# Kernel tuning notes

Measured on AMD Instinct MI355X. Metric: run time of the kernel, lower is better.

The kernel has to match this reference:

```python
import jax, jax.numpy as jnp
import numpy as np

N_BINS = 15
DELTA = 1.0 / N_BINS


def setup_inputs() -> dict:
    key = jax.random.key(0)
    k1, k2 = jax.random.split(key)
    N, C = 4_000_000, 10
    # scale 5 -> confident softmax -> low collision entropy so bins [0,1) are populated
    logits = jax.random.normal(k1, (N, C), dtype=jnp.float32) * 5.0
    labels = jax.random.randint(k2, (N,), 0, C)
    return {"logits": logits, "labels": labels}


def reference(logits, labels):
    # probs: [N, C]
    probs = jax.nn.softmax(logits, axis=-1)
    # collision entropy H2 per sample: [N]
    u = -jnp.log2(jnp.sum(probs * probs, axis=-1) + 1e-12)
    err_real = (jnp.argmax(probs, axis=-1) != labels).astype(jnp.float32)  # [N]

    n = u.shape[0]
    # bin b covers [b*DELTA, (b+1)*DELTA); samples with u outside [0,1) go to overflow bin
    bin_idx = jnp.floor(u / DELTA).astype(jnp.int32)
    valid = (u >= 0.0) & (u < 1.0)
    seg = jnp.where(valid, bin_idx, N_BINS)

    vf = valid.astype(jnp.float32)
    counts = jax.ops.segment_sum(vf, seg, num_segments=N_BINS + 1)[:N_BINS]
    sum_u = jax.ops.segment_sum(jnp.where(valid, u, 0.0), seg, num_segments=N_BINS + 1)[:N_BINS]
    sum_err = jax.ops.segment_sum(jnp.where(valid, err_real, 0.0), seg, num_segments=N_BINS + 1)[:N_BINS]

    pi = counts / n                      # population weight per bin
    nonempty = counts > 0
    cnt = jnp.where(nonempty, counts, 1.0)
    u_b = sum_u / cnt                    # mean H2 in bin
    err_b = sum_err / cnt                # empirical error rate in bin

    # risk-from-H2 reference curve
    inner = jnp.clip(2.0 * jnp.exp2(-u_b) - 1.0, 0.0, None)
    r_ref = 0.5 * (1.0 - jnp.sqrt(inner))

    gaps = jnp.where(nonempty, jnp.abs(err_b - r_ref) * pi, 0.0)
    return jnp.sum(gaps)
```

## Files before the change

kernel.cpp:

```cpp
#include <hip/hip_runtime.h>
#include <math.h>
#include <stdint.h>

#define NB 15
#define TROWS 512
#define TBYTES (TROWS * 40)
#define LBYTES (TROWS * 4)
#define NCOPY 8
#define ACCSTRIDE 64


__device__ __forceinline__ void gload_lds16(const void* g, void* ldsBase, uint32_t ldsByteOff)
{
    __builtin_amdgcn_global_load_lds(
        (const __attribute__((address_space(1))) uint32_t*)g,
        (__attribute__((address_space(3))) uint32_t*)((char*)ldsBase + ldsByteOff),
        16, 0, 0);
}

__device__ __forceinline__ void gload_lds4(const void* g, void* ldsBase, uint32_t ldsByteOff)
{
    __builtin_amdgcn_global_load_lds(
        (const __attribute__((address_space(1))) uint32_t*)g,
        (__attribute__((address_space(3))) uint32_t*)((char*)ldsBase + ldsByteOff),
        4, 0, 0);
}

__device__ __forceinline__ void row_stats(const float lv[10], float lvl_lab, bool rowOK,
                                          int& bin, float& u, int& e10)
{
    float m = lv[0];
#pragma unroll
    for (int j = 1; j < 10; ++j) m = fmaxf(m, lv[j]);

    const float c = 1.44269504088896340736f;
    float mc = m * c;
    float Z = 0.0f, S = 0.0f;
#pragma unroll
    for (int j = 0; j < 10; ++j) {
        float e = exp2f(fmaf(lv[j], c, -mc));
        Z += e;
        S = fmaf(e, e, S);
    }
    float ratio = S * __builtin_amdgcn_rcpf(Z * Z);
    u = -log2f(ratio + 1e-12f);

    bool valid = rowOK && (u >= 0.0f) && (u < 1.0f);
    bin = -1;
    if (valid) {
        bin = (int)(u * 15.0f);
        if (bin > 14) bin = 14;
    }
    if (!valid) u = 0.0f;
    e10 = (lvl_lab != m) ? 1 : 0;
}

__global__ __launch_bounds__(256) void bin_kernel(
    const float* __restrict__ logits,
    const int* __restrict__ labels,
    float* __restrict__ acc,
    int N, int numTiles)
{
    __shared__ float ldsLog[2][TROWS * 10];
    __shared__ int   ldsLab[2][TROWS];
    __shared__ float s_acc[3 * NB];

    const int t = threadIdx.x;
    if (t < 3 * NB) s_acc[t] = 0.0f;
    const int wid  = t >> 6;
    const int lane = t & 63;

    int   pk[NB];
    float su[NB];
#pragma unroll
    for (int b = 0; b < NB; ++b) { pk[b] = 0; su[b] = 0.0f; }

    const char* srcB = (const char*)logits;
    const char* labB = (const char*)labels;
    const long long totB  = (long long)N * 40;
    const long long ltotB = (long long)N * 4;

    auto stage = [&](int buf, long long tl) {
#pragma unroll
        for (int k = 0; k < 5; ++k) {
            uint32_t loff = (uint32_t)(wid * 5 + k) << 10;
            long long gb = tl * TBYTES + loff + lane * 16;
            if (gb > totB - 16) gb = totB - 16;
            gload_lds16(srcB + gb, &ldsLog[buf][0], __builtin_amdgcn_readfirstlane(loff));
        }
#pragma unroll
        for (int k = 0; k < 2; ++k) {
            uint32_t loff = (uint32_t)(wid * 2 + k) << 8;
            long long gb = tl * LBYTES + loff + lane * 4;
            if (gb > ltotB - 4) gb = ltotB - 4;
            gload_lds4(labB + gb, &ldsLab[buf][0], __builtin_amdgcn_readfirstlane(loff));
        }
    };

    long long tile = blockIdx.x;
    stage(0, tile);
    int cur = 0;

    for (; tile < numTiles; tile += gridDim.x) {
        const long long nxt = tile + gridDim.x;
        const bool hasNext = (nxt < numTiles);
        if (hasNext) {
            stage(cur ^ 1, nxt);
            asm volatile("s_waitcnt vmcnt(7)" ::: "memory");
        } else {
            asm volatile("s_waitcnt vmcnt(0)" ::: "memory");
        }
        __builtin_amdgcn_s_barrier();

        const float* L  = ldsLog[cur];
        const int*   LB = ldsLab[cur];

        const int r0 = (int)tile * TROWS + t;
        const int r1 = r0 + 256;
        int lab0 = LB[t];       lab0 = lab0 < 0 ? 0 : (lab0 > 9 ? 9 : lab0);
        int lab1 = LB[t + 256]; lab1 = lab1 < 0 ? 0 : (lab1 > 9 ? 9 : lab1);

        float a[10], b2[10];
        {
            const float2* p = (const float2*)(L + t * 10);
#pragma unroll
            for (int j = 0; j < 5; ++j) { float2 w = p[j]; a[2*j] = w.x; a[2*j+1] = w.y; }
        }
        {
            const float2* p = (const float2*)(L + (t + 256) * 10);
#pragma unroll
            for (int j = 0; j < 5; ++j) { float2 w = p[j]; b2[2*j] = w.x; b2[2*j+1] = w.y; }
        }
        float lvl0 = L[t * 10 + lab0];
        float lvl1 = L[(t + 256) * 10 + lab1];

        int binA, eA, binB, eB;
        float uA, uB;
        row_stats(a,  lvl0, r0 < N, binA, uA, eA);
        row_stats(b2, lvl1, r1 < N, binB, uB, eB);

        int incA = 1 + (eA << 16);
        int incB = 1 + (eB << 16);
#pragma unroll
        for (int b = 0; b < NB; ++b) {
            bool mA = (binA == b);
            bool mB = (binB == b);
            pk[b] += (mA ? incA : 0) + (mB ? incB : 0);
            su[b] += (mA ? uA : 0.0f) + (mB ? uB : 0.0f);
        }

        asm volatile("s_waitcnt lgkmcnt(0)" ::: "memory");
        __builtin_amdgcn_s_barrier();
        cur ^= 1;
    }

#pragma unroll
    for (int b = 0; b < NB; ++b) {
        int   p = pk[b];
        float s = su[b];
#pragma unroll
        for (int off = 1; off < 64; off <<= 1) {
            p += __shfl_xor(p, off, 64);
            s += __shfl_xor(s, off, 64);
        }
        if (lane == 0) {
            atomicAdd(&s_acc[b],          (float)(p & 0xFFFF));
            atomicAdd(&s_acc[NB + b],     s);
            atomicAdd(&s_acc[2 * NB + b], (float)(p >> 16));
        }
    }
    __syncthreads();
    if (t < 3 * NB) {
        float v = s_acc[t];
        if (v != 0.0f)
            atomicAdd(&acc[(blockIdx.x & (NCOPY - 1)) * ACCSTRIDE + t], v);
    }
}

__global__ void finalize_kernel(const float* __restrict__ acc,
                                float* __restrict__ out, float n)
{
    int b = threadIdx.x;
    float gap = 0.0f;
    if (b < NB) {
        float cnt = 0.0f, sumu = 0.0f, serr = 0.0f;
#pragma unroll
        for (int c = 0; c < NCOPY; ++c) {
            cnt  += acc[c * ACCSTRIDE + b];
            sumu += acc[c * ACCSTRIDE + NB + b];
            serr += acc[c * ACCSTRIDE + 2 * NB + b];
        }
        if (cnt > 0.0f) {
            float u_b   = sumu / cnt;
            float err_b = serr / cnt;
            float inner = 2.0f * exp2f(-u_b) - 1.0f;
            if (inner < 0.0f) inner = 0.0f;
            float r_ref = 0.5f * (1.0f - sqrtf(inner));
            gap = fabsf(err_b - r_ref) * (cnt / n);
        }
    }
#pragma unroll
    for (int off = 32; off >= 1; off >>= 1)
        gap += __shfl_xor(gap, off, 64);
    if (b == 0) out[0] = gap;
}

extern "C" void kernel_launch(void* const* d_in, const int* in_sizes, int n_in,
                              void* d_out, int out_size, void* d_ws, size_t ws_size,
                              hipStream_t stream)
{
    const float* logits = (const float*)d_in[0];
    const int*   labels = (const int*)d_in[1];
    const int N = in_sizes[1];

    float* acc = (float*)d_ws;
    hipMemsetAsync(acc, 0, NCOPY * ACCSTRIDE * sizeof(float), stream);

    const int numTiles = (N + TROWS - 1) / TROWS;
    int blocks = numTiles < 768 ? numTiles : 768;
    bin_kernel<<<blocks, 256, 0, stream>>>(logits, labels, acc, N, numTiles);
    finalize_kernel<<<1, 64, 0, stream>>>(acc, (float*)d_out, (float)N);
}
```

Measured before the change: 242.2 us.

## Replace LDS double-buffered staging with direct per-thread global loads

Removes the global_load_lds double-buffered tile staging and the per-tile barriers. Each thread now reads its own row straight from global memory with strided float2 loads in a grid-stride loop, and the label logit is picked with selects instead of an indexed LDS read. The grid grows from 768 to 1024 blocks. This drops the barrier and LDS overhead, but each thread's row reads are 40-byte strided and less coalesced, and there is no explicit prefetch.

```diff
diff --git a/kernel.cpp b/kernel.cpp
--- a/kernel.cpp
+++ b/kernel.cpp
@@ -3,71 +3,20 @@
 #include <stdint.h>
 
 #define NB 15
-#define TROWS 512
-#define TBYTES (TROWS * 40)
-#define LBYTES (TROWS * 4)
 #define NCOPY 8
 #define ACCSTRIDE 64
 
 
-__device__ __forceinline__ void gload_lds16(const void* g, void* ldsBase, uint32_t ldsByteOff)
-{
-    __builtin_amdgcn_global_load_lds(
-        (const __attribute__((address_space(1))) uint32_t*)g,
-        (__attribute__((address_space(3))) uint32_t*)((char*)ldsBase + ldsByteOff),
-        16, 0, 0);
-}
-
-__device__ __forceinline__ void gload_lds4(const void* g, void* ldsBase, uint32_t ldsByteOff)
-{
-    __builtin_amdgcn_global_load_lds(
-        (const __attribute__((address_space(1))) uint32_t*)g,
-        (__attribute__((address_space(3))) uint32_t*)((char*)ldsBase + ldsByteOff),
-        4, 0, 0);
-}
-
-__device__ __forceinline__ void row_stats(const float lv[10], float lvl_lab, bool rowOK,
-                                          int& bin, float& u, int& e10)
-{
-    float m = lv[0];
-#pragma unroll
-    for (int j = 1; j < 10; ++j) m = fmaxf(m, lv[j]);
-
-    const float c = 1.44269504088896340736f;
-    float mc = m * c;
-    float Z = 0.0f, S = 0.0f;
-#pragma unroll
-    for (int j = 0; j < 10; ++j) {
-        float e = exp2f(fmaf(lv[j], c, -mc));
-        Z += e;
-        S = fmaf(e, e, S);
-    }
-    float ratio = S * __builtin_amdgcn_rcpf(Z * Z);
-    u = -log2f(ratio + 1e-12f);
-
-    bool valid = rowOK && (u >= 0.0f) && (u < 1.0f);
-    bin = -1;
-    if (valid) {
-        bin = (int)(u * 15.0f);
-        if (bin > 14) bin = 14;
-    }
-    if (!valid) u = 0.0f;
-    e10 = (lvl_lab != m) ? 1 : 0;
-}
-
 __global__ __launch_bounds__(256) void bin_kernel(
     const float* __restrict__ logits,
     const int* __restrict__ labels,
-    float* __restrict__ acc,
-    int N, int numTiles)
+    float* __restrict__ acc, int N)
 {
-    __shared__ float ldsLog[2][TROWS * 10];
-    __shared__ int   ldsLab[2][TROWS];
     __shared__ float s_acc[3 * NB];
-
     const int t = threadIdx.x;
     if (t < 3 * NB) s_acc[t] = 0.0f;
-    const int wid  = t >> 6;
+    __syncthreads();
+
     const int lane = t & 63;
 
     int   pk[NB];
@@ -75,83 +24,51 @@
 #pragma unroll
     for (int b = 0; b < NB; ++b) { pk[b] = 0; su[b] = 0.0f; }
 
-    const char* srcB = (const char*)logits;
-    const char* labB = (const char*)labels;
-    const long long totB  = (long long)N * 40;
-    const long long ltotB = (long long)N * 4;
+    const long long stride = (long long)gridDim.x * 256;
 
-    auto stage = [&](int buf, long long tl) {
+    for (long long r = (long long)blockIdx.x * 256 + t; r < N; r += stride) {
+        const float2* p = (const float2*)(logits + r * 10);
+        float lv[10];
 #pragma unroll
-        for (int k = 0; k < 5; ++k) {
-            uint32_t loff = (uint32_t)(wid * 5 + k) << 10;
-            long long gb = tl * TBYTES + loff + lane * 16;
-            if (gb > totB - 16) gb = totB - 16;
-            gload_lds16(srcB + gb, &ldsLog[buf][0], __builtin_amdgcn_readfirstlane(loff));
+        for (int j = 0; j < 5; ++j) { float2 w = p[j]; lv[2*j] = w.x; lv[2*j+1] = w.y; }
+        const int lab = labels[r];
+
+        float lvl = lv[0];
+#pragma unroll
+        for (int j = 1; j < 10; ++j) lvl = (lab == j) ? lv[j] : lvl;
+
+        float m = lv[0];
+#pragma unroll
+        for (int j = 1; j < 10; ++j) m = fmaxf(m, lv[j]);
+
+        const float c = 1.44269504088896340736f;
+        float mc = m * c;
+        float Z = 0.0f, S = 0.0f;
+#pragma unroll
+        for (int j = 0; j < 10; ++j) {
+            float e = exp2f(fmaf(lv[j], c, -mc));
+            Z += e;
+            S = fmaf(e, e, S);
         }
-#pragma unroll
-        for (int k = 0; k < 2; ++k) {
-            uint32_t loff = (uint32_t)(wid * 2 + k) << 8;
-            long long gb = tl * LBYTES + loff + lane * 4;
-            if (gb > ltotB - 4) gb = ltotB - 4;
-            gload_lds4(labB + gb, &ldsLab[buf][0], __builtin_amdgcn_readfirstlane(loff));
+        float ratio = S * __builtin_amdgcn_rcpf(Z * Z);
+        float u = -log2f(ratio + 1e-12f);
+
+        bool valid = (u >= 0.0f) && (u < 1.0f);
+        int bin = -1;
+        if (valid) {
+            bin = (int)(u * 15.0f);
+            if (bin > 14) bin = 14;
         }
-    };
+        if (!valid) u = 0.0f;
+        int e10 = (lvl != m) ? 1 : 0;
+        int inc = 1 + (e10 << 16);
 
-    long long tile = blockIdx.x;
-    stage(0, tile);
-    int cur = 0;
-
-    for (; tile < numTiles; tile += gridDim.x) {
-        const long long nxt = tile + gridDim.x;
-        const bool hasNext = (nxt < numTiles);
-        if (hasNext) {
-            stage(cur ^ 1, nxt);
-            asm volatile("s_waitcnt vmcnt(7)" ::: "memory");
-        } else {
-            asm volatile("s_waitcnt vmcnt(0)" ::: "memory");
-        }
-        __builtin_amdgcn_s_barrier();
-
-        const float* L  = ldsLog[cur];
-        const int*   LB = ldsLab[cur];
-
-        const int r0 = (int)tile * TROWS + t;
-        const int r1 = r0 + 256;
-        int lab0 = LB[t];       lab0 = lab0 < 0 ? 0 : (lab0 > 9 ? 9 : lab0);
-        int lab1 = LB[t + 256]; lab1 = lab1 < 0 ? 0 : (lab1 > 9 ? 9 : lab1);
-
-        float a[10], b2[10];
-        {
-            const float2* p = (const float2*)(L + t * 10);
-#pragma unroll
-            for (int j = 0; j < 5; ++j) { float2 w = p[j]; a[2*j] = w.x; a[2*j+1] = w.y; }
-        }
-        {
-            const float2* p = (const float2*)(L + (t + 256) * 10);
-#pragma unroll
-            for (int j = 0; j < 5; ++j) { float2 w = p[j]; b2[2*j] = w.x; b2[2*j+1] = w.y; }
-        }
-        float lvl0 = L[t * 10 + lab0];
-        float lvl1 = L[(t + 256) * 10 + lab1];
-
-        int binA, eA, binB, eB;
-        float uA, uB;
-        row_stats(a,  lvl0, r0 < N, binA, uA, eA);
-        row_stats(b2, lvl1, r1 < N, binB, uB, eB);
-
-        int incA = 1 + (eA << 16);
-        int incB = 1 + (eB << 16);
 #pragma unroll
         for (int b = 0; b < NB; ++b) {
-            bool mA = (binA == b);
-            bool mB = (binB == b);
-            pk[b] += (mA ? incA : 0) + (mB ? incB : 0);
-            su[b] += (mA ? uA : 0.0f) + (mB ? uB : 0.0f);
+            bool mb = (bin == b);
+            pk[b] += mb ? inc : 0;
+            su[b] += mb ? u : 0.0f;
         }
-
-        asm volatile("s_waitcnt lgkmcnt(0)" ::: "memory");
-        __builtin_amdgcn_s_barrier();
-        cur ^= 1;
     }
 
 #pragma unroll
@@ -216,8 +133,9 @@
     float* acc = (float*)d_ws;
     hipMemsetAsync(acc, 0, NCOPY * ACCSTRIDE * sizeof(float), stream);
 
-    const int numTiles = (N + TROWS - 1) / TROWS;
-    int blocks = numTiles < 768 ? numTiles : 768;
-    bin_kernel<<<blocks, 256, 0, stream>>>(logits, labels, acc, N, numTiles);
+    int blocks = (N + 255) / 256;
+    if (blocks > 1024) blocks = 1024;
+    if (blocks < 1) blocks = 1;
+    bin_kernel<<<blocks, 256, 0, stream>>>(logits, labels, acc, N);
     finalize_kernel<<<1, 64, 0, stream>>>(acc, (float*)d_out, (float)N);
 }
```

New measurement: 242.8 us. Within noise of the previous version (+0.3%).
